# Optimization experiments

Measured on AMD Instinct MI355X. Metric: run time of the kernel, lower is better.

The kernel has to match this reference:

```python
import jax, jax.numpy as jnp
import numpy as np

B, N_TOK, N_ATOM = 1, 1024, 4096
C_S, C_Z, C_ATOM, C_PAIR = 384, 128, 128, 16
N_QUERY, N_KEY = 32, 128
N_BLOCKS = N_ATOM // N_QUERY
EPS = 1e-5


def layer_norm_scale(x, w):
    # LayerNorm with create_offset=False (scale only)
    mu = jnp.mean(x, axis=-1, keepdims=True)
    var = jnp.mean(jnp.square(x - mu), axis=-1, keepdims=True)
    return (x - mu) * jax.lax.rsqrt(var + EPS) * w


def atom_to_token_idx(num_atoms):
    # num_atoms: [N_tok] int -> token index for each atom [N_ATOM]
    ends = jnp.cumsum(num_atoms)
    return jnp.searchsorted(ends, jnp.arange(N_ATOM), side='right')


def setup_inputs() -> dict:
    key = jax.random.key(0)
    ks = jax.random.split(key, 10)
    return {
        'token_mask': jnp.ones((B, N_TOK), jnp.float32),
        'num_atoms_per_token': jnp.full((B, N_TOK), N_ATOM // N_TOK, jnp.int32),
        'cl': jax.random.normal(ks[0], (B, N_ATOM, C_ATOM), jnp.float32),
        'plm': jax.random.normal(ks[1], (B, N_BLOCKS, N_QUERY, N_KEY, C_PAIR), jnp.float32),
        'si_trunk': jax.random.normal(ks[2], (B, N_TOK, C_S), jnp.float32),
        'zij_trunk': jax.random.normal(ks[3], (B, N_TOK, N_TOK, C_Z), jnp.float32),
        'rl': jax.random.normal(ks[4], (B, N_ATOM, 3), jnp.float32),
        'ln_s_w': jnp.ones((C_S,), jnp.float32),
        'W_s': jax.random.normal(ks[5], (C_S, C_ATOM), jnp.float32) * 0.02,
        'b_s': jnp.zeros((C_ATOM,), jnp.float32),
        'ln_z_w': jnp.ones((C_Z,), jnp.float32),
        'W_z': jax.random.normal(ks[6], (C_Z, C_PAIR), jnp.float32) * 0.02,
        'b_z': jnp.zeros((C_PAIR,), jnp.float32),
        'W_r': jax.random.normal(ks[7], (3, C_ATOM), jnp.float32) * 0.02,
        'b_r': jnp.zeros((C_ATOM,), jnp.float32),
        'n_query': N_QUERY,
        'n_key': N_KEY,
    }


def reference(token_mask, num_atoms_per_token, cl, plm, si_trunk, zij_trunk, rl,
              ln_s_w, W_s, b_s, ln_z_w, W_z, b_z, W_r, b_r, n_query, n_key):
    # --- single rep: LayerNorm + Linear, then token -> atom broadcast ---
    s = jnp.einsum('btc,cd->btd', layer_norm_scale(si_trunk, ln_s_w), W_s) + b_s
    s = s * token_mask[..., None]  # zero padded tokens
    tok = jax.vmap(atom_to_token_idx)(num_atoms_per_token)  # [B, N_ATOM]
    s_atoms = jnp.take_along_axis(s, tok[..., None], axis=1)  # [B, N_ATOM, c_atom]
    cl_out = cl + s_atoms

    # --- pair rep: LayerNorm + Linear, then pair -> local block gather ---
    z = jnp.einsum('bijc,cd->bijd', layer_norm_scale(zij_trunk, ln_z_w), W_z) + b_z
    n_blocks = N_ATOM // n_query
    q_idx = jnp.arange(n_blocks)[:, None] * n_query + jnp.arange(n_query)[None, :]
    k_off = n_query // 2 - n_key // 2  # key window centered on query block
    k_idx = jnp.arange(n_blocks)[:, None] * n_query + k_off + jnp.arange(n_key)[None, :]
    valid = ((k_idx >= 0) & (k_idx < N_ATOM)).astype(z.dtype)  # [L, n_key]
    k_idx_c = jnp.clip(k_idx, 0, N_ATOM - 1)
    tok_q = tok[:, q_idx]    # [B, L, n_query]
    tok_k = tok[:, k_idx_c]  # [B, L, n_key]

    def gather_blocks(zb, tq, tk):
        return zb[tq[:, :, None], tk[:, None, :]]  # [L, nq, nk, C_PAIR]

    z_blk = jax.vmap(gather_blocks)(z, tok_q, tok_k)
    z_blk = z_blk * valid[None, :, None, :, None]
    plm_out = plm + z_blk

    # --- noisy position projection ---
    ql = cl_out + jnp.einsum('bac,cd->bad', rl, W_r) + b_r
    return cl_out, plm_out, ql
```

## Files before the change

### kernel.cpp

```cpp
#include <hip/hip_runtime.h>

#define N_TOKS 1024
#define N_ATOMS 4096
#define CS 384
#define CZ 128
#define CATOM 128
#define CPAIR 16
#define NQ 32
#define NK 128
#define NBLK 128
#define KOFF (-48)
#define KSEG 32
#define NSEG (NK / KSEG)
#define NTILE (NBLK * NSEG)
#define NB_A 256
#define MAXP 1024
#define MAPSTRIDE 68
#define LN_EPS 1e-5f

union alignas(16) SMem {
    struct {
        int ends[N_TOKS];
        int tokq[NQ]; int tokk[KSEG];
        int qmap[NQ]; int kmap[KSEG];
        int uqtok[NQ]; int uktok[KSEG];
        int uqk[2];
        int wsum[4];
        int vmask;
    } b;
    struct {
        float xh[CS][4];
        float sacc[8][4][CATOM];
        float s_l[4][CATOM];
        int ends[N_TOKS];
        int wsum[4];
    } a;
};

__device__ __forceinline__ void scan_ends(const int* __restrict__ na, int* ends, int* wsum, int t) {
    int4 v = ((const int4*)na)[t];
    int e0 = v.x, e1 = e0 + v.y, e2 = e1 + v.z, e3 = e2 + v.w;
    int s = e3;
    int lane = t & 63, w = t >> 6;
    #pragma unroll
    for (int off = 1; off < 64; off <<= 1) {
        int u = __shfl_up(s, off);
        if (lane >= off) s += u;
    }
    if (lane == 63) wsum[w] = s;
    __syncthreads();
    int wbase = 0;
    #pragma unroll
    for (int i = 0; i < 4; i++) wbase += (i < w) ? wsum[i] : 0;
    int base = wbase + s - e3;
    ends[4 * t + 0] = base + e0;
    ends[4 * t + 1] = base + e1;
    ends[4 * t + 2] = base + e2;
    ends[4 * t + 3] = base + e3;
    __syncthreads();
}

__device__ __forceinline__ int bsearch_tok(const int* ends, int a) {
    int lo = 0, hi = N_TOKS - 1;
    while (lo < hi) { int mid = (lo + hi) >> 1; if (ends[mid] > a) hi = mid; else lo = mid + 1; }
    return lo;
}

__global__ __launch_bounds__(256) void k_pre(
        const int* __restrict__ na, const float* __restrict__ si,
        const float* __restrict__ lnw, const float* __restrict__ Ws,
        const float* __restrict__ bs, const float* __restrict__ mask,
        const float* __restrict__ cl, const float* __restrict__ rl,
        const float* __restrict__ Wr, const float* __restrict__ br,
        const float* __restrict__ zij, const float* __restrict__ lnzw,
        const float* __restrict__ Wz, const float* __restrict__ bz,
        float* __restrict__ z_ws, int* __restrict__ maps_ws,
        float* __restrict__ cl_out, float* __restrict__ ql) {
    __shared__ SMem sm;
    int t = threadIdx.x;
    int x = blockIdx.x;

    if (x >= NTILE) {
        int b = x - NTILE, Tlo = b * 4;
        scan_ends(na, sm.a.ends, sm.a.wsum, t);
        {
            int tl = t >> 6, l = t & 63;
            const float4* row4 = (const float4*)(si + (size_t)(Tlo + tl) * CS);
            float4 v0 = row4[l];
            float4 v1 = make_float4(0.f, 0.f, 0.f, 0.f);
            if (l < 32) v1 = row4[64 + l];
            float sum = v0.x + v0.y + v0.z + v0.w + v1.x + v1.y + v1.z + v1.w;
            float sq = v0.x*v0.x + v0.y*v0.y + v0.z*v0.z + v0.w*v0.w
                     + v1.x*v1.x + v1.y*v1.y + v1.z*v1.z + v1.w*v1.w;
            #pragma unroll
            for (int m = 32; m >= 1; m >>= 1) { sum += __shfl_xor(sum, m); sq += __shfl_xor(sq, m); }
            float mu = sum * (1.f / CS);
            float rstd = rsqrtf(sq * (1.f / CS) - mu * mu + LN_EPS);
            float4 g0 = ((const float4*)lnw)[l];
            sm.a.xh[4*l+0][tl] = (v0.x - mu) * rstd * g0.x;
            sm.a.xh[4*l+1][tl] = (v0.y - mu) * rstd * g0.y;
            sm.a.xh[4*l+2][tl] = (v0.z - mu) * rstd * g0.z;
            sm.a.xh[4*l+3][tl] = (v0.w - mu) * rstd * g0.w;
            if (l < 32) {
                float4 g1 = ((const float4*)lnw)[64 + l];
                sm.a.xh[256+4*l+0][tl] = (v1.x - mu) * rstd * g1.x;
                sm.a.xh[256+4*l+1][tl] = (v1.y - mu) * rstd * g1.y;
                sm.a.xh[256+4*l+2][tl] = (v1.z - mu) * rstd * g1.z;
                sm.a.xh[256+4*l+3][tl] = (v1.w - mu) * rstd * g1.w;
            }
        }
        __syncthreads();
        {
            int d4 = t & 31, cc = t >> 5;
            float4 a0 = make_float4(0,0,0,0), a1 = a0, a2 = a0, a3 = a0;
            const float4* Ws4 = (const float4*)Ws;
            int c0 = 48 * cc;
            #pragma unroll 4
            for (int c = c0; c < c0 + 48; c++) {
                float4 w = Ws4[(size_t)c * 32 + d4];
                float4 xv = *(const float4*)&sm.a.xh[c][0];
                a0.x += xv.x * w.x; a0.y += xv.x * w.y; a0.z += xv.x * w.z; a0.w += xv.x * w.w;
                a1.x += xv.y * w.x; a1.y += xv.y * w.y; a1.z += xv.y * w.z; a1.w += xv.y * w.w;
                a2.x += xv.z * w.x; a2.y += xv.z * w.y; a2.z += xv.z * w.z; a2.w += xv.z * w.w;
                a3.x += xv.w * w.x; a3.y += xv.w * w.y; a3.z += xv.w * w.z; a3.w += xv.w * w.w;
            }
            *(float4*)&sm.a.sacc[cc][0][d4 * 4] = a0;
            *(float4*)&sm.a.sacc[cc][1][d4 * 4] = a1;
            *(float4*)&sm.a.sacc[cc][2][d4 * 4] = a2;
            *(float4*)&sm.a.sacc[cc][3][d4 * 4] = a3;
        }
        __syncthreads();
        if (t < 128) {
            int tk = t >> 5, d = t & 31;
            float4 a = make_float4(0,0,0,0);
            #pragma unroll
            for (int cc = 0; cc < 8; cc++) {
                float4 p = *(const float4*)&sm.a.sacc[cc][tk][d * 4];
                a.x += p.x; a.y += p.y; a.z += p.z; a.w += p.w;
            }
            float4 bb = ((const float4*)bs)[d];
            float m = mask[Tlo + tk];
            a.x = (a.x + bb.x) * m; a.y = (a.y + bb.y) * m;
            a.z = (a.z + bb.z) * m; a.w = (a.w + bb.w) * m;
            *(float4*)&sm.a.s_l[tk][d * 4] = a;
        }
        __syncthreads();
        int elo = (Tlo == 0) ? 0 : sm.a.ends[Tlo - 1];
        int e_0 = sm.a.ends[Tlo], e_1 = sm.a.ends[Tlo + 1], e_2 = sm.a.ends[Tlo + 2];
        int ehi = (b == NB_A - 1) ? N_ATOMS : sm.a.ends[Tlo + 3];
        elo = min(max(elo, 0), N_ATOMS);
        ehi = min(max(ehi, 0), N_ATOMS);
        if (ehi < elo) ehi = elo;
        int items = (ehi - elo) * 32;
        for (int i = t; i < items; i += 256) {
            int a = elo + (i >> 5), d = i & 31;
            int tk = (a >= e_0) + (a >= e_1) + (a >= e_2);
            float4 c4 = ((const float4*)cl)[(size_t)a * 32 + d];
            float4 sv = *(const float4*)&sm.a.s_l[tk][d * 4];
            float4 co;
            co.x = c4.x + sv.x; co.y = c4.y + sv.y; co.z = c4.z + sv.z; co.w = c4.w + sv.w;
            float px = rl[a * 3 + 0], py = rl[a * 3 + 1], pz = rl[a * 3 + 2];
            float4 w0 = ((const float4*)Wr)[d];
            float4 w1 = ((const float4*)Wr)[32 + d];
            float4 w2 = ((const float4*)Wr)[64 + d];
            float4 bb = ((const float4*)br)[d];
            float4 q;
            q.x = co.x + px * w0.x + py * w1.x + pz * w2.x + bb.x;
            q.y = co.y + px * w0.y + py * w1.y + pz * w2.y + bb.y;
            q.z = co.z + px * w0.z + py * w1.z + pz * w2.z + bb.z;
            q.w = co.w + px * w0.w + py * w1.w + pz * w2.w + bb.w;
            ((float4*)cl_out)[(size_t)a * 32 + d] = co;
            ((float4*)ql)[(size_t)a * 32 + d] = q;
        }
        return;
    }

    int blk = x >> 2, kseg = x & 3;
    scan_ends(na, sm.b.ends, sm.b.wsum, t);

    if (t < NQ) {
        sm.b.tokq[t] = bsearch_tok(sm.b.ends, blk * NQ + t);
    } else if (t >= 64 && t < 64 + KSEG) {
        int kk = t - 64;
        int kg = blk * NQ + KOFF + kseg * KSEG + kk;
        bool val = (kg >= 0 && kg < N_ATOMS);
        unsigned long long vm = __ballot(val);
        if (kk == 0) sm.b.vmask = (int)(vm & 0xffffffffull);
        sm.b.tokk[kk] = bsearch_tok(sm.b.ends, min(max(kg, 0), N_ATOMS - 1));
    }
    __syncthreads();

    if (t < NQ) {
        int tq = sm.b.tokq[t];
        bool head = (t == 0) || (tq != sm.b.tokq[t - 1]);
        unsigned long long m = __ballot(head);
        int rank = (int)__popcll(m & ((2ull << t) - 1)) - 1;
        sm.b.qmap[t] = rank;
        if (head) sm.b.uqtok[rank] = tq;
        if (t == 0) sm.b.uqk[0] = (int)__popcll(m);
    } else if (t >= 64 && t < 64 + KSEG) {
        int lane = t - 64;
        int tk = sm.b.tokk[lane];
        bool head = (lane == 0) || (tk != sm.b.tokk[lane - 1]);
        unsigned long long m = __ballot(head);
        int rank = (int)__popcll(m & ((2ull << lane) - 1)) - 1;
        sm.b.kmap[lane] = rank;
        if (head) sm.b.uktok[rank] = tk;
        if (lane == 0) sm.b.uqk[1] = (int)__popcll(m);
    }
    __syncthreads();
    int uq = sm.b.uqk[0], uk = sm.b.uqk[1];
    int npairs = uq * uk;

    int* mp = maps_ws + x * MAPSTRIDE;
    if (t < NQ) mp[1 + t] = sm.b.qmap[t];
    else if (t >= 64 && t < 64 + KSEG) mp[33 + (t - 64)] = sm.b.kmap[t - 64];
    else if (t == 96) mp[0] = uk;
    else if (t == 97) mp[65] = sm.b.vmask;

    for (int p = t; p < npairs; p += 256) {
        int qi = p / uk, ki = p - qi * uk;
        int tq = sm.b.uqtok[qi], tk = sm.b.uktok[ki];
        const float* row = zij + ((size_t)tq * N_TOKS + tk) * CZ;
        float sum = 0.f, sq = 0.f;
        for (int c4 = 0; c4 < CZ / 4; c4++) {
            float4 v = *(const float4*)(row + c4 * 4);
            sum += v.x + v.y + v.z + v.w;
            sq  += v.x * v.x + v.y * v.y + v.z * v.z + v.w * v.w;
        }
        float mu = sum * (1.f / CZ);
        float rstd = rsqrtf(sq * (1.f / CZ) - mu * mu + LN_EPS);
        float acc[CPAIR];
        #pragma unroll
        for (int d = 0; d < CPAIR; d++) acc[d] = bz[d];
        for (int c4 = 0; c4 < CZ / 4; c4++) {
            float4 v = *(const float4*)(row + c4 * 4);
            float xs4[4] = {v.x, v.y, v.z, v.w};
            #pragma unroll
            for (int j = 0; j < 4; j++) {
                int c = c4 * 4 + j;
                float xv = (xs4[j] - mu) * rstd * lnzw[c];
                const float* wrow = Wz + c * CPAIR;
                #pragma unroll
                for (int d = 0; d < CPAIR; d++) acc[d] += xv * wrow[d];
            }
        }
        float4* zt = (float4*)(z_ws + ((size_t)x * MAXP + p) * CPAIR);
        zt[0] = make_float4(acc[0], acc[1], acc[2], acc[3]);
        zt[1] = make_float4(acc[4], acc[5], acc[6], acc[7]);
        zt[2] = make_float4(acc[8], acc[9], acc[10], acc[11]);
        zt[3] = make_float4(acc[12], acc[13], acc[14], acc[15]);
    }
}

__global__ __launch_bounds__(256) void k_stream(
        const float* __restrict__ z_ws, const int* __restrict__ maps_ws,
        const float* __restrict__ plm, float* __restrict__ plm_out) {
    __shared__ int qmap_l[8];
    __shared__ int kmap_l[32];
    __shared__ int s_uk, s_vm;
    int t = threadIdx.x;
    int b = blockIdx.x;
    int tau = b >> 2, qq = b & 3;
    int blk = tau >> 2, kseg = tau & 3;

    const int* mp = maps_ws + tau * MAPSTRIDE;
    if (t < 32) kmap_l[t] = mp[33 + t];
    else if (t < 40) qmap_l[t - 32] = mp[1 + qq * 8 + (t - 32)];
    else if (t == 40) s_uk = mp[0];
    else if (t == 41) s_vm = mp[65];
    __syncthreads();
    int uk = s_uk, vm = s_vm;

    const float4* plm4 = (const float4*)plm;
    const float4* z4 = (const float4*)z_ws;
    float4* out4 = (float4*)plm_out;
    #pragma unroll
    for (int i = 0; i < 4; i++) {
        int f = t + i * 256;
        int d4 = f & 3;
        int kk = (f >> 2) & 31;
        int q  = f >> 7;
        int grow = blk * NQ + qq * 8 + q;
        size_t g = ((size_t)grow * NK + kseg * KSEG + kk) * 4 + d4;
        float4 v = plm4[g];
        int pidx = qmap_l[q] * uk + kmap_l[kk];
        float4 z = z4[((size_t)tau * MAXP + pidx) * 4 + d4];
        float vd = ((vm >> kk) & 1) ? 1.0f : 0.0f;
        v.x += vd * z.x; v.y += vd * z.y; v.z += vd * z.z; v.w += vd * z.w;
        out4[g] = v;
    }
}

extern "C" void kernel_launch(void* const* d_in, const int* in_sizes, int n_in,
                              void* d_out, int out_size, void* d_ws, size_t ws_size,
                              hipStream_t stream) {
    (void)in_sizes; (void)n_in; (void)out_size; (void)ws_size;
    const float* token_mask = (const float*)d_in[0];
    const int*   num_atoms  = (const int*)d_in[1];
    const float* cl   = (const float*)d_in[2];
    const float* plm  = (const float*)d_in[3];
    const float* si   = (const float*)d_in[4];
    const float* zij  = (const float*)d_in[5];
    const float* rl   = (const float*)d_in[6];
    const float* ln_s_w = (const float*)d_in[7];
    const float* W_s  = (const float*)d_in[8];
    const float* b_s  = (const float*)d_in[9];
    const float* ln_z_w = (const float*)d_in[10];
    const float* W_z  = (const float*)d_in[11];
    const float* b_z  = (const float*)d_in[12];
    const float* W_r  = (const float*)d_in[13];
    const float* b_r  = (const float*)d_in[14];

    float* out_cl  = (float*)d_out;
    float* out_plm = out_cl + (size_t)N_ATOMS * CATOM;
    float* out_ql  = out_plm + (size_t)NBLK * NQ * NK * CPAIR;

    float* z_ws    = (float*)d_ws;
    int*   maps_ws = (int*)((char*)d_ws + (size_t)NTILE * MAXP * CPAIR * 4);

    k_pre<<<NTILE + NB_A, 256, 0, stream>>>(num_atoms, si, ln_s_w, W_s, b_s, token_mask,
                                            cl, rl, W_r, b_r,
                                            zij, ln_z_w, W_z, b_z,
                                            z_ws, maps_ws, out_cl, out_ql);
    k_stream<<<NTILE * 4, 256, 0, stream>>>(z_ws, maps_ws, plm, out_plm);
}
```

Measured before the change: 35.53 us.

## Compute pair projection once per query block over full key window

Each query block now computes the unique token-pair LayerNorm+projection over its whole 128-key window in one workgroup, instead of splitting the window into four 32-key segments handled by separate workgroups. Tokens shared at segment boundaries are no longer recomputed, and the number of pre-kernel workgroups for the pair path drops from 512 to 128. In exchange each workgroup handles more pairs serially, so there is less parallelism in the compute-heavy phase. The stream kernel indexes the per-block maps by segment instead.

New measurement: 38.15 us. 7.4% more time.

```diff
diff --git a/kernel.cpp b/kernel.cpp
--- a/kernel.cpp
+++ b/kernel.cpp
@@ -11,22 +11,21 @@
 #define NBLK 128
 #define KOFF (-48)
 #define KSEG 32
-#define NSEG (NK / KSEG)
-#define NTILE (NBLK * NSEG)
+#define KWIN 128
 #define NB_A 256
-#define MAXP 1024
-#define MAPSTRIDE 68
+#define MAXP 4096
+#define MAPSTRIDE 168
 #define LN_EPS 1e-5f
 
 union alignas(16) SMem {
     struct {
         int ends[N_TOKS];
-        int tokq[NQ]; int tokk[KSEG];
-        int qmap[NQ]; int kmap[KSEG];
-        int uqtok[NQ]; int uktok[KSEG];
+        int tokq[NQ]; int tokk[KWIN];
+        int qmap[NQ]; int kmap[KWIN];
+        int uqtok[NQ]; int uktok[KWIN];
+        int vmask[4];
         int uqk[2];
         int wsum[4];
-        int vmask;
     } b;
     struct {
         float xh[CS][4];
@@ -80,8 +79,8 @@
     int t = threadIdx.x;
     int x = blockIdx.x;
 
-    if (x >= NTILE) {
-        int b = x - NTILE, Tlo = b * 4;
+    if (x >= NBLK) {
+        int b = x - NBLK, Tlo = b * 4;
         scan_ends(na, sm.a.ends, sm.a.wsum, t);
         {
             int tl = t >> 6, l = t & 63;
@@ -175,18 +174,25 @@
         return;
     }
 
-    int blk = x >> 2, kseg = x & 3;
+    int blk = x;
     scan_ends(na, sm.b.ends, sm.b.wsum, t);
 
     if (t < NQ) {
         sm.b.tokq[t] = bsearch_tok(sm.b.ends, blk * NQ + t);
-    } else if (t >= 64 && t < 64 + KSEG) {
-        int kk = t - 64;
-        int kg = blk * NQ + KOFF + kseg * KSEG + kk;
-        bool val = (kg >= 0 && kg < N_ATOMS);
-        unsigned long long vm = __ballot(val);
-        if (kk == 0) sm.b.vmask = (int)(vm & 0xffffffffull);
-        sm.b.tokk[kk] = bsearch_tok(sm.b.ends, min(max(kg, 0), N_ATOMS - 1));
+    } else if (t >= 64 && t < 128) {
+        int l = t - 64;
+        int kg0 = blk * NQ + KOFF + l;
+        int kg1 = kg0 + 64;
+        sm.b.tokk[l]      = bsearch_tok(sm.b.ends, min(max(kg0, 0), N_ATOMS - 1));
+        sm.b.tokk[l + 64] = bsearch_tok(sm.b.ends, min(max(kg1, 0), N_ATOMS - 1));
+        unsigned long long v0 = __ballot(kg0 >= 0 && kg0 < N_ATOMS);
+        unsigned long long v1 = __ballot(kg1 >= 0 && kg1 < N_ATOMS);
+        if (l == 0) {
+            sm.b.vmask[0] = (int)(v0 & 0xffffffffull);
+            sm.b.vmask[1] = (int)(v0 >> 32);
+            sm.b.vmask[2] = (int)(v1 & 0xffffffffull);
+            sm.b.vmask[3] = (int)(v1 >> 32);
+        }
     }
     __syncthreads();
 
@@ -198,25 +204,32 @@
         sm.b.qmap[t] = rank;
         if (head) sm.b.uqtok[rank] = tq;
         if (t == 0) sm.b.uqk[0] = (int)__popcll(m);
-    } else if (t >= 64 && t < 64 + KSEG) {
-        int lane = t - 64;
-        int tk = sm.b.tokk[lane];
-        bool head = (lane == 0) || (tk != sm.b.tokk[lane - 1]);
-        unsigned long long m = __ballot(head);
-        int rank = (int)__popcll(m & ((2ull << lane) - 1)) - 1;
-        sm.b.kmap[lane] = rank;
-        if (head) sm.b.uktok[rank] = tk;
-        if (lane == 0) sm.b.uqk[1] = (int)__popcll(m);
+    } else if (t >= 64 && t < 128) {
+        int l = t - 64;
+        int tk0 = sm.b.tokk[l];
+        bool h0 = (l == 0) || (tk0 != sm.b.tokk[l - 1]);
+        unsigned long long m0 = __ballot(h0);
+        int r0 = (int)__popcll(m0 & ((2ull << l) - 1)) - 1;
+        sm.b.kmap[l] = r0;
+        if (h0) sm.b.uktok[r0] = tk0;
+        int carry = (int)__popcll(m0);
+        int tk1 = sm.b.tokk[l + 64];
+        bool h1 = (tk1 != sm.b.tokk[l + 63]);
+        unsigned long long m1 = __ballot(h1);
+        int r1 = carry + (int)__popcll(m1 & ((2ull << l) - 1)) - 1;
+        sm.b.kmap[l + 64] = r1;
+        if (h1) sm.b.uktok[r1] = tk1;
+        if (l == 0) sm.b.uqk[1] = carry + (int)__popcll(m1);
     }
     __syncthreads();
     int uq = sm.b.uqk[0], uk = sm.b.uqk[1];
     int npairs = uq * uk;
 
-    int* mp = maps_ws + x * MAPSTRIDE;
+    int* mp = maps_ws + blk * MAPSTRIDE;
     if (t < NQ) mp[1 + t] = sm.b.qmap[t];
-    else if (t >= 64 && t < 64 + KSEG) mp[33 + (t - 64)] = sm.b.kmap[t - 64];
-    else if (t == 96) mp[0] = uk;
-    else if (t == 97) mp[65] = sm.b.vmask;
+    else if (t == 32) mp[0] = uk;
+    else if (t >= 33 && t < 37) mp[161 + (t - 33)] = sm.b.vmask[t - 33];
+    else if (t >= 64 && t < 192) mp[33 + (t - 64)] = sm.b.kmap[t - 64];
 
     for (int p = t; p < npairs; p += 256) {
         int qi = p / uk, ki = p - qi * uk;
@@ -245,7 +258,7 @@
                 for (int d = 0; d < CPAIR; d++) acc[d] += xv * wrow[d];
             }
         }
-        float4* zt = (float4*)(z_ws + ((size_t)x * MAXP + p) * CPAIR);
+        float4* zt = (float4*)(z_ws + ((size_t)blk * MAXP + p) * CPAIR);
         zt[0] = make_float4(acc[0], acc[1], acc[2], acc[3]);
         zt[1] = make_float4(acc[4], acc[5], acc[6], acc[7]);
         zt[2] = make_float4(acc[8], acc[9], acc[10], acc[11]);
@@ -261,14 +274,13 @@
     __shared__ int s_uk, s_vm;
     int t = threadIdx.x;
     int b = blockIdx.x;
-    int tau = b >> 2, qq = b & 3;
-    int blk = tau >> 2, kseg = tau & 3;
-
-    const int* mp = maps_ws + tau * MAPSTRIDE;
-    if (t < 32) kmap_l[t] = mp[33 + t];
+    int blk = b >> 4, kseg = (b >> 2) & 3, qq = b & 3;
+
+    const int* mp = maps_ws + blk * MAPSTRIDE;
+    if (t < 32) kmap_l[t] = mp[33 + kseg * KSEG + t];
     else if (t < 40) qmap_l[t - 32] = mp[1 + qq * 8 + (t - 32)];
     else if (t == 40) s_uk = mp[0];
-    else if (t == 41) s_vm = mp[65];
+    else if (t == 41) s_vm = mp[161 + kseg];
     __syncthreads();
     int uk = s_uk, vm = s_vm;
 
@@ -285,7 +297,7 @@
         size_t g = ((size_t)grow * NK + kseg * KSEG + kk) * 4 + d4;
         float4 v = plm4[g];
         int pidx = qmap_l[q] * uk + kmap_l[kk];
-        float4 z = z4[((size_t)tau * MAXP + pidx) * 4 + d4];
+        float4 z = z4[((size_t)blk * MAXP + pidx) * 4 + d4];
         float vd = ((vm >> kk) & 1) ? 1.0f : 0.0f;
         v.x += vd * z.x; v.y += vd * z.y; v.z += vd * z.z; v.w += vd * z.w;
         out4[g] = v;
@@ -317,11 +329,11 @@
     float* out_ql  = out_plm + (size_t)NBLK * NQ * NK * CPAIR;
 
     float* z_ws    = (float*)d_ws;
-    int*   maps_ws = (int*)((char*)d_ws + (size_t)NTILE * MAXP * CPAIR * 4);
-
-    k_pre<<<NTILE + NB_A, 256, 0, stream>>>(num_atoms, si, ln_s_w, W_s, b_s, token_mask,
-                                            cl, rl, W_r, b_r,
-                                            zij, ln_z_w, W_z, b_z,
-                                            z_ws, maps_ws, out_cl, out_ql);
-    k_stream<<<NTILE * 4, 256, 0, stream>>>(z_ws, maps_ws, plm, out_plm);
-}
+    int*   maps_ws = (int*)((char*)d_ws + (size_t)NBLK * MAXP * CPAIR * 4);
+
+    k_pre<<<NBLK + NB_A, 256, 0, stream>>>(num_atoms, si, ln_s_w, W_s, b_s, token_mask,
+                                           cl, rl, W_r, b_r,
+                                           zij, ln_z_w, W_z, b_z,
+                                           z_ws, maps_ws, out_cl, out_ql);
+    k_stream<<<NBLK * 16, 256, 0, stream>>>(z_ws, maps_ws, plm, out_plm);
+}
```

## Move single-rep work into stream kernel and use nontemporal plm loads/stores

Applied to the files above, without the earlier changes.

The single-representation path (LayerNorm+Linear of si, cl_out and ql) moves from the first kernel into the second, plm-streaming kernel. The first kernel now does only the pair LayerNorm/projection, which makes it shorter and lets the second kernel's extra blocks run alongside the plm traffic. The plm streaming loop also issues all four loads before any compute and uses nontemporal load/store builtins to avoid polluting the cache. The risk is a larger LDS footprint in k_stream from the union, which may lower occupancy for the streaming blocks.

New measurement: 40.66 us. +14.4%, slower.

```diff
diff --git a/kernel.cpp b/kernel.cpp
--- a/kernel.cpp
+++ b/kernel.cpp
@@ -14,20 +14,29 @@
 #define NSEG (NK / KSEG)
 #define NTILE (NBLK * NSEG)
 #define NB_A 256
+#define NB_S (NTILE * 4)
 #define MAXP 1024
 #define MAPSTRIDE 68
 #define LN_EPS 1e-5f
 
-union alignas(16) SMem {
+typedef float f32x4 __attribute__((ext_vector_type(4)));
+
+struct alignas(16) SMemB {
+    int ends[N_TOKS];
+    int tokq[NQ]; int tokk[KSEG];
+    int qmap[NQ]; int kmap[KSEG];
+    int uqtok[NQ]; int uktok[KSEG];
+    int uqk[2];
+    int wsum[4];
+    int vmask;
+};
+
+union alignas(16) SMemS {
     struct {
-        int ends[N_TOKS];
-        int tokq[NQ]; int tokk[KSEG];
-        int qmap[NQ]; int kmap[KSEG];
-        int uqtok[NQ]; int uktok[KSEG];
-        int uqk[2];
-        int wsum[4];
-        int vmask;
-    } b;
+        int qmap_l[8];
+        int kmap_l[32];
+        int uk; int vm;
+    } s;
     struct {
         float xh[CS][4];
         float sacc[8][4][CATOM];
@@ -67,21 +76,105 @@
 }
 
 __global__ __launch_bounds__(256) void k_pre(
+        const int* __restrict__ na,
+        const float* __restrict__ zij, const float* __restrict__ lnzw,
+        const float* __restrict__ Wz, const float* __restrict__ bz,
+        float* __restrict__ z_ws, int* __restrict__ maps_ws) {
+    __shared__ SMemB sm;
+    int t = threadIdx.x;
+    int x = blockIdx.x;
+    int blk = x >> 2, kseg = x & 3;
+    scan_ends(na, sm.ends, sm.wsum, t);
+
+    if (t < NQ) {
+        sm.tokq[t] = bsearch_tok(sm.ends, blk * NQ + t);
+    } else if (t >= 64 && t < 64 + KSEG) {
+        int kk = t - 64;
+        int kg = blk * NQ + KOFF + kseg * KSEG + kk;
+        unsigned long long vm = __ballot(kg >= 0 && kg < N_ATOMS);
+        if (kk == 0) sm.vmask = (int)(vm & 0xffffffffull);
+        sm.tokk[kk] = bsearch_tok(sm.ends, min(max(kg, 0), N_ATOMS - 1));
+    }
+    __syncthreads();
+
+    if (t < NQ) {
+        int tq = sm.tokq[t];
+        bool head = (t == 0) || (tq != sm.tokq[t - 1]);
+        unsigned long long m = __ballot(head);
+        int rank = (int)__popcll(m & ((2ull << t) - 1)) - 1;
+        sm.qmap[t] = rank;
+        if (head) sm.uqtok[rank] = tq;
+        if (t == 0) sm.uqk[0] = (int)__popcll(m);
+    } else if (t >= 64 && t < 64 + KSEG) {
+        int lane = t - 64;
+        int tk = sm.tokk[lane];
+        bool head = (lane == 0) || (tk != sm.tokk[lane - 1]);
+        unsigned long long m = __ballot(head);
+        int rank = (int)__popcll(m & ((2ull << lane) - 1)) - 1;
+        sm.kmap[lane] = rank;
+        if (head) sm.uktok[rank] = tk;
+        if (lane == 0) sm.uqk[1] = (int)__popcll(m);
+    }
+    __syncthreads();
+    int uq = sm.uqk[0], uk = sm.uqk[1];
+    int npairs = uq * uk;
+
+    int* mp = maps_ws + x * MAPSTRIDE;
+    if (t < NQ) mp[1 + t] = sm.qmap[t];
+    else if (t >= 64 && t < 64 + KSEG) mp[33 + (t - 64)] = sm.kmap[t - 64];
+    else if (t == 96) mp[0] = uk;
+    else if (t == 97) mp[65] = sm.vmask;
+
+    for (int p = t; p < npairs; p += 256) {
+        int qi = p / uk, ki = p - qi * uk;
+        int tq = sm.uqtok[qi], tk = sm.uktok[ki];
+        const float* row = zij + ((size_t)tq * N_TOKS + tk) * CZ;
+        float sum = 0.f, sq = 0.f;
+        for (int c4 = 0; c4 < CZ / 4; c4++) {
+            float4 v = *(const float4*)(row + c4 * 4);
+            sum += v.x + v.y + v.z + v.w;
+            sq  += v.x * v.x + v.y * v.y + v.z * v.z + v.w * v.w;
+        }
+        float mu = sum * (1.f / CZ);
+        float rstd = rsqrtf(sq * (1.f / CZ) - mu * mu + LN_EPS);
+        float acc[CPAIR];
+        #pragma unroll
+        for (int d = 0; d < CPAIR; d++) acc[d] = bz[d];
+        for (int c4 = 0; c4 < CZ / 4; c4++) {
+            float4 v = *(const float4*)(row + c4 * 4);
+            float xs4[4] = {v.x, v.y, v.z, v.w};
+            #pragma unroll
+            for (int j = 0; j < 4; j++) {
+                int c = c4 * 4 + j;
+                float xv = (xs4[j] - mu) * rstd * lnzw[c];
+                const float* wrow = Wz + c * CPAIR;
+                #pragma unroll
+                for (int d = 0; d < CPAIR; d++) acc[d] += xv * wrow[d];
+            }
+        }
+        float4* zt = (float4*)(z_ws + ((size_t)x * MAXP + p) * CPAIR);
+        zt[0] = make_float4(acc[0], acc[1], acc[2], acc[3]);
+        zt[1] = make_float4(acc[4], acc[5], acc[6], acc[7]);
+        zt[2] = make_float4(acc[8], acc[9], acc[10], acc[11]);
+        zt[3] = make_float4(acc[12], acc[13], acc[14], acc[15]);
+    }
+}
+
+__global__ __launch_bounds__(256) void k_stream(
+        const float* __restrict__ z_ws, const int* __restrict__ maps_ws,
+        const float* __restrict__ plm, float* __restrict__ plm_out,
         const int* __restrict__ na, const float* __restrict__ si,
         const float* __restrict__ lnw, const float* __restrict__ Ws,
         const float* __restrict__ bs, const float* __restrict__ mask,
         const float* __restrict__ cl, const float* __restrict__ rl,
         const float* __restrict__ Wr, const float* __restrict__ br,
-        const float* __restrict__ zij, const float* __restrict__ lnzw,
-        const float* __restrict__ Wz, const float* __restrict__ bz,
-        float* __restrict__ z_ws, int* __restrict__ maps_ws,
         float* __restrict__ cl_out, float* __restrict__ ql) {
-    __shared__ SMem sm;
+    __shared__ SMemS sm;
     int t = threadIdx.x;
     int x = blockIdx.x;
 
-    if (x >= NTILE) {
-        int b = x - NTILE, Tlo = b * 4;
+    if (x >= NB_S) {
+        int b = x - NB_S, Tlo = b * 4;
         scan_ends(na, sm.a.ends, sm.a.wsum, t);
         {
             int tl = t >> 6, l = t & 63;
@@ -175,106 +268,23 @@
         return;
     }
 
-    int blk = x >> 2, kseg = x & 3;
-    scan_ends(na, sm.b.ends, sm.b.wsum, t);
-
-    if (t < NQ) {
-        sm.b.tokq[t] = bsearch_tok(sm.b.ends, blk * NQ + t);
-    } else if (t >= 64 && t < 64 + KSEG) {
-        int kk = t - 64;
-        int kg = blk * NQ + KOFF + kseg * KSEG + kk;
-        bool val = (kg >= 0 && kg < N_ATOMS);
-        unsigned long long vm = __ballot(val);
-        if (kk == 0) sm.b.vmask = (int)(vm & 0xffffffffull);
-        sm.b.tokk[kk] = bsearch_tok(sm.b.ends, min(max(kg, 0), N_ATOMS - 1));
-    }
-    __syncthreads();
-
-    if (t < NQ) {
-        int tq = sm.b.tokq[t];
-        bool head = (t == 0) || (tq != sm.b.tokq[t - 1]);
-        unsigned long long m = __ballot(head);
-        int rank = (int)__popcll(m & ((2ull << t) - 1)) - 1;
-        sm.b.qmap[t] = rank;
-        if (head) sm.b.uqtok[rank] = tq;
-        if (t == 0) sm.b.uqk[0] = (int)__popcll(m);
-    } else if (t >= 64 && t < 64 + KSEG) {
-        int lane = t - 64;
-        int tk = sm.b.tokk[lane];
-        bool head = (lane == 0) || (tk != sm.b.tokk[lane - 1]);
-        unsigned long long m = __ballot(head);
-        int rank = (int)__popcll(m & ((2ull << lane) - 1)) - 1;
-        sm.b.kmap[lane] = rank;
-        if (head) sm.b.uktok[rank] = tk;
-        if (lane == 0) sm.b.uqk[1] = (int)__popcll(m);
-    }
-    __syncthreads();
-    int uq = sm.b.uqk[0], uk = sm.b.uqk[1];
-    int npairs = uq * uk;
-
-    int* mp = maps_ws + x * MAPSTRIDE;
-    if (t < NQ) mp[1 + t] = sm.b.qmap[t];
-    else if (t >= 64 && t < 64 + KSEG) mp[33 + (t - 64)] = sm.b.kmap[t - 64];
-    else if (t == 96) mp[0] = uk;
-    else if (t == 97) mp[65] = sm.b.vmask;
-
-    for (int p = t; p < npairs; p += 256) {
-        int qi = p / uk, ki = p - qi * uk;
-        int tq = sm.b.uqtok[qi], tk = sm.b.uktok[ki];
-        const float* row = zij + ((size_t)tq * N_TOKS + tk) * CZ;
-        float sum = 0.f, sq = 0.f;
-        for (int c4 = 0; c4 < CZ / 4; c4++) {
-            float4 v = *(const float4*)(row + c4 * 4);
-            sum += v.x + v.y + v.z + v.w;
-            sq  += v.x * v.x + v.y * v.y + v.z * v.z + v.w * v.w;
-        }
-        float mu = sum * (1.f / CZ);
-        float rstd = rsqrtf(sq * (1.f / CZ) - mu * mu + LN_EPS);
-        float acc[CPAIR];
-        #pragma unroll
-        for (int d = 0; d < CPAIR; d++) acc[d] = bz[d];
-        for (int c4 = 0; c4 < CZ / 4; c4++) {
-            float4 v = *(const float4*)(row + c4 * 4);
-            float xs4[4] = {v.x, v.y, v.z, v.w};
-            #pragma unroll
-            for (int j = 0; j < 4; j++) {
-                int c = c4 * 4 + j;
-                float xv = (xs4[j] - mu) * rstd * lnzw[c];
-                const float* wrow = Wz + c * CPAIR;
-                #pragma unroll
-                for (int d = 0; d < CPAIR; d++) acc[d] += xv * wrow[d];
-            }
-        }
-        float4* zt = (float4*)(z_ws + ((size_t)x * MAXP + p) * CPAIR);
-        zt[0] = make_float4(acc[0], acc[1], acc[2], acc[3]);
-        zt[1] = make_float4(acc[4], acc[5], acc[6], acc[7]);
-        zt[2] = make_float4(acc[8], acc[9], acc[10], acc[11]);
-        zt[3] = make_float4(acc[12], acc[13], acc[14], acc[15]);
-    }
-}
-
-__global__ __launch_bounds__(256) void k_stream(
-        const float* __restrict__ z_ws, const int* __restrict__ maps_ws,
-        const float* __restrict__ plm, float* __restrict__ plm_out) {
-    __shared__ int qmap_l[8];
-    __shared__ int kmap_l[32];
-    __shared__ int s_uk, s_vm;
-    int t = threadIdx.x;
-    int b = blockIdx.x;
-    int tau = b >> 2, qq = b & 3;
+    int tau = x >> 2, qq = x & 3;
     int blk = tau >> 2, kseg = tau & 3;
 
     const int* mp = maps_ws + tau * MAPSTRIDE;
-    if (t < 32) kmap_l[t] = mp[33 + t];
-    else if (t < 40) qmap_l[t - 32] = mp[1 + qq * 8 + (t - 32)];
-    else if (t == 40) s_uk = mp[0];
-    else if (t == 41) s_vm = mp[65];
-    __syncthreads();
-    int uk = s_uk, vm = s_vm;
-
-    const float4* plm4 = (const float4*)plm;
+    if (t < 32) sm.s.kmap_l[t] = mp[33 + t];
+    else if (t < 40) sm.s.qmap_l[t - 32] = mp[1 + qq * 8 + (t - 32)];
+    else if (t == 40) sm.s.uk = mp[0];
+    else if (t == 41) sm.s.vm = mp[65];
+    __syncthreads();
+    int uk = sm.s.uk, vm = sm.s.vm;
+
+    const f32x4* plm4 = (const f32x4*)plm;
     const float4* z4 = (const float4*)z_ws;
-    float4* out4 = (float4*)plm_out;
+    f32x4* out4 = (f32x4*)plm_out;
+
+    size_t gs[4];
+    f32x4 pv[4];
     #pragma unroll
     for (int i = 0; i < 4; i++) {
         int f = t + i * 256;
@@ -282,13 +292,21 @@
         int kk = (f >> 2) & 31;
         int q  = f >> 7;
         int grow = blk * NQ + qq * 8 + q;
-        size_t g = ((size_t)grow * NK + kseg * KSEG + kk) * 4 + d4;
-        float4 v = plm4[g];
-        int pidx = qmap_l[q] * uk + kmap_l[kk];
+        gs[i] = ((size_t)grow * NK + kseg * KSEG + kk) * 4 + d4;
+        pv[i] = __builtin_nontemporal_load(&plm4[gs[i]]);
+    }
+    #pragma unroll
+    for (int i = 0; i < 4; i++) {
+        int f = t + i * 256;
+        int d4 = f & 3;
+        int kk = (f >> 2) & 31;
+        int q  = f >> 7;
+        int pidx = sm.s.qmap_l[q] * uk + sm.s.kmap_l[kk];
         float4 z = z4[((size_t)tau * MAXP + pidx) * 4 + d4];
         float vd = ((vm >> kk) & 1) ? 1.0f : 0.0f;
+        f32x4 v = pv[i];
         v.x += vd * z.x; v.y += vd * z.y; v.z += vd * z.z; v.w += vd * z.w;
-        out4[g] = v;
+        __builtin_nontemporal_store(v, &out4[gs[i]]);
     }
 }
 
@@ -319,9 +337,8 @@
     float* z_ws    = (float*)d_ws;
     int*   maps_ws = (int*)((char*)d_ws + (size_t)NTILE * MAXP * CPAIR * 4);
 
-    k_pre<<<NTILE + NB_A, 256, 0, stream>>>(num_atoms, si, ln_s_w, W_s, b_s, token_mask,
-                                            cl, rl, W_r, b_r,
-                                            zij, ln_z_w, W_z, b_z,
-                                            z_ws, maps_ws, out_cl, out_ql);
-    k_stream<<<NTILE * 4, 256, 0, stream>>>(z_ws, maps_ws, plm, out_plm);
-}
+    k_pre<<<NTILE, 256, 0, stream>>>(num_atoms, zij, ln_z_w, W_z, b_z, z_ws, maps_ws);
+    k_stream<<<NB_S + NB_A, 256, 0, stream>>>(z_ws, maps_ws, plm, out_plm,
+                                              num_atoms, si, ln_s_w, W_s, b_s, token_mask,
+                                              cl, rl, W_r, b_r, out_cl, out_ql);
+}
```
